# Performance work log

Measured on AMD Instinct MI355X. Metric: run time of the kernel, lower is better.

## Reference

```python
import jax, jax.numpy as jnp
import numpy as np

N_NODES = 50000
N_EDGES = 600000
IN_DIM = 128
HID = 256
OUT = 3


def setup_inputs() -> dict:
    key = jax.random.key(0)
    ks = jax.random.split(key, 10)
    x = jax.random.normal(ks[0], (N_NODES, IN_DIM), dtype=jnp.float32)
    edge_index = jax.random.randint(ks[1], (2, N_EDGES), 0, N_NODES, dtype=jnp.int64)
    s = lambda k, shp: jax.random.normal(k, shp, dtype=jnp.float32) * (1.0 / np.sqrt(shp[0]))
    return {
        "x": x,
        "edge_index": edge_index,
        # SAGEConv1: lin_l (applied to aggregated neighbors, with bias), lin_r (root, no bias)
        "W1l": s(ks[2], (IN_DIM, HID)), "b1": jnp.zeros((HID,), jnp.float32), "W1r": s(ks[3], (IN_DIM, HID)),
        # SAGEConv2
        "W2l": s(ks[4], (HID, HID)), "b2": jnp.zeros((HID,), jnp.float32), "W2r": s(ks[5], (HID, HID)),
        # classification head
        "Wh": s(ks[6], (HID, OUT)), "bh": jnp.zeros((OUT,), jnp.float32),
    }


def _sage_conv(x, edge_index, Wl, b, Wr):
    """PyG SAGEConv with mean aggregation: out = lin_l(mean_{j->i} x_j) + lin_r(x_i)."""
    src, dst = edge_index[0], edge_index[1]
    n = x.shape[0]
    # gather source features and scatter-mean onto targets
    msg_sum = jax.ops.segment_sum(x[src], dst, num_segments=n)          # [N, d]
    deg = jax.ops.segment_sum(jnp.ones((src.shape[0],), x.dtype), dst, num_segments=n)
    mean = msg_sum / jnp.maximum(deg, 1.0)[:, None]                      # isolated nodes -> 0
    return mean @ Wl + b + x @ Wr


def reference(x, edge_index, W1l, b1, W1r, W2l, b2, W2r, Wh, bh):
    h = jax.nn.relu(_sage_conv(x, edge_index, W1l, b1, W1r))
    # dropout(p=0.2) is identity in eval mode
    h = jax.nn.relu(_sage_conv(h, edge_index, W2l, b2, W2r))
    return h @ Wh + bh
```

## Files before the change

kernel.cpp:

```cpp
#include <hip/hip_runtime.h>
#include <hip/hip_bf16.h>

#define N_NODES 50000
#define N_EDGES 600000
#define IN_DIM 128
#define HID 256
#define OUT_DIM 3

#define M_PAD 50048

#define SCAN_B 256
#define SCAN_NB ((N_NODES + SCAN_B - 1) / SCAN_B)

typedef __bf16 bf16x8 __attribute__((ext_vector_type(8)));
typedef float f32x4 __attribute__((ext_vector_type(4)));

static __device__ __forceinline__ unsigned short f2b(float f) {
    union { float f; unsigned u; } u; u.f = f;
    unsigned r = u.u + 0x7fffu + ((u.u >> 16) & 1u);
    return (unsigned short)(r >> 16);
}
static __device__ __forceinline__ float b2f(unsigned short b) {
    union { unsigned u; float f; } u; u.u = ((unsigned)b) << 16;
    return u.f;
}


__global__ void count_deg_kernel(const int* __restrict__ dst, int* __restrict__ counts) {
    int e = blockIdx.x * blockDim.x + threadIdx.x;
    if (e < N_EDGES) atomicAdd(&counts[dst[e]], 1);
}

__global__ __launch_bounds__(256) void block_sum_kernel(const int* __restrict__ counts,
                                                        int* __restrict__ partial) {
    int node = blockIdx.x * SCAN_B + threadIdx.x;
    int v = (node < N_NODES) ? counts[node] : 0;
#pragma unroll
    for (int off = 32; off > 0; off >>= 1) v += __shfl_down(v, off);
    __shared__ int ws[4];
    if ((threadIdx.x & 63) == 0) ws[threadIdx.x >> 6] = v;
    __syncthreads();
    if (threadIdx.x == 0) partial[blockIdx.x] = ws[0] + ws[1] + ws[2] + ws[3];
}

__global__ __launch_bounds__(256) void scan_partial_kernel(int* __restrict__ partial) {
    __shared__ int s[SCAN_B];
    int t = threadIdx.x;
    int v = (t < SCAN_NB) ? partial[t] : 0;
    s[t] = v;
    __syncthreads();
    for (int off = 1; off < SCAN_B; off <<= 1) {
        int u = (t >= off) ? s[t - off] : 0;
        __syncthreads();
        s[t] += u;
        __syncthreads();
    }
    if (t < SCAN_NB) partial[t] = s[t] - v;
}

__global__ __launch_bounds__(256) void write_rowptr_kernel(const int* __restrict__ counts,
                                                           const int* __restrict__ partial,
                                                           int* __restrict__ row_ptr) {
    __shared__ int s[SCAN_B];
    int t = threadIdx.x;
    int node = blockIdx.x * SCAN_B + t;
    int v = (node < N_NODES) ? counts[node] : 0;
    s[t] = v;
    __syncthreads();
    for (int off = 1; off < SCAN_B; off <<= 1) {
        int u = (t >= off) ? s[t - off] : 0;
        __syncthreads();
        s[t] += u;
        __syncthreads();
    }
    if (node < N_NODES) row_ptr[node] = partial[blockIdx.x] + s[t] - v;
    if (node == 0) row_ptr[N_NODES] = N_EDGES;
}

__global__ void fill_csr_kernel(const int* __restrict__ src, const int* __restrict__ dst,
                                const int* __restrict__ row_ptr, int* __restrict__ cursor,
                                int* __restrict__ csr_src) {
    int e = blockIdx.x * blockDim.x + threadIdx.x;
    if (e < N_EDGES) {
        int d = dst[e];
        int pos = atomicAdd(&cursor[d], 1);
        csr_src[row_ptr[d] + pos] = src[e];
    }
}


__global__ void cast_f2b_kernel(const float* __restrict__ in, unsigned short* __restrict__ out, int n) {
    int i = blockIdx.x * blockDim.x + threadIdx.x;
    if (i * 4 < n) {
        float4 v = ((const float4*)in)[i];
        ushort4 o;
        o.x = f2b(v.x); o.y = f2b(v.y); o.z = f2b(v.z); o.w = f2b(v.w);
        ((ushort4*)out)[i] = o;
    }
}

__global__ void tcast4_kernel(const float* __restrict__ W1l, const float* __restrict__ W1r,
                              const float* __restrict__ W2l, const float* __restrict__ W2r,
                              unsigned short* __restrict__ W1lt, unsigned short* __restrict__ W1rt,
                              unsigned short* __restrict__ W2lt, unsigned short* __restrict__ W2rt) {
    int i = blockIdx.x * blockDim.x + threadIdx.x;
    const float* in; unsigned short* out; int K, base;
    if (i < 32768)        { in = W1l; out = W1lt; K = IN_DIM; base = 0; }
    else if (i < 65536)   { in = W1r; out = W1rt; K = IN_DIM; base = 32768; }
    else if (i < 131072)  { in = W2l; out = W2lt; K = HID;    base = 65536; }
    else if (i < 196608)  { in = W2r; out = W2rt; K = HID;    base = 131072; }
    else return;
    int j = i - base;
    int k = j >> 8;
    int n = j & 255;
    out[(size_t)n * K + k] = f2b(in[j]);
}

__global__ void init_out_kernel(const float* __restrict__ bh, float* __restrict__ out) {
    int i = blockIdx.x * blockDim.x + threadIdx.x;
    if (i < N_NODES * 3) out[i] = bh[i % 3];
}


static __device__ __forceinline__ void addv(float* acc, uint4 v) {
    acc[0] += b2f((unsigned short)(v.x & 0xffff));
    acc[1] += b2f((unsigned short)(v.x >> 16));
    acc[2] += b2f((unsigned short)(v.y & 0xffff));
    acc[3] += b2f((unsigned short)(v.y >> 16));
    acc[4] += b2f((unsigned short)(v.z & 0xffff));
    acc[5] += b2f((unsigned short)(v.z >> 16));
    acc[6] += b2f((unsigned short)(v.w & 0xffff));
    acc[7] += b2f((unsigned short)(v.w >> 16));
}

static __device__ __forceinline__ uint4 pack8(const float* a) {
    uint4 pk;
    pk.x = (unsigned)f2b(a[0]) | ((unsigned)f2b(a[1]) << 16);
    pk.y = (unsigned)f2b(a[2]) | ((unsigned)f2b(a[3]) << 16);
    pk.z = (unsigned)f2b(a[4]) | ((unsigned)f2b(a[5]) << 16);
    pk.w = (unsigned)f2b(a[6]) | ((unsigned)f2b(a[7]) << 16);
    return pk;
}

__global__ __launch_bounds__(256) void agg_mean256_kernel(const unsigned short* __restrict__ feat,
                                                          const int* __restrict__ row_ptr,
                                                          const int* __restrict__ csr_src,
                                                          unsigned short* __restrict__ out) {
    int node = blockIdx.x * 4 + (threadIdx.x >> 6);
    if (node >= N_NODES) return;
    int lane = threadIdx.x & 63;
    int half = lane >> 5, lh = lane & 31;
    const uint4* f4 = (const uint4*)feat;
    float acc[8];
#pragma unroll
    for (int j = 0; j < 8; j++) acc[j] = 0.f;
    int beg = row_ptr[node], end = row_ptr[node + 1];
    int i = beg;
    for (; i + 4 <= end; i += 4) {
        int sA = csr_src[i + half];
        int sB = csr_src[i + 2 + half];
        uint4 vA = f4[(size_t)sA * 32 + lh];
        uint4 vB = f4[(size_t)sB * 32 + lh];
        addv(acc, vA);
        addv(acc, vB);
    }
    if (i + 2 <= end) {
        int s = csr_src[i + half];
        addv(acc, f4[(size_t)s * 32 + lh]);
        i += 2;
    }
    if (i < end && half == 0) {
        int s = csr_src[i];
        addv(acc, f4[(size_t)s * 32 + lh]);
    }
    float inv = (end > beg) ? 1.0f / (float)(end - beg) : 0.0f;
#pragma unroll
    for (int j = 0; j < 8; j++) {
        acc[j] += __shfl_xor(acc[j], 32);
        acc[j] *= inv;
    }
    if (half == 0) ((uint4*)(out + (size_t)node * 256))[lh] = pack8(acc);
}

__global__ __launch_bounds__(256) void agg_mean128_kernel(const unsigned short* __restrict__ feat,
                                                          const int* __restrict__ row_ptr,
                                                          const int* __restrict__ csr_src,
                                                          unsigned short* __restrict__ out) {
    int node = blockIdx.x * 4 + (threadIdx.x >> 6);
    if (node >= N_NODES) return;
    int lane = threadIdx.x & 63;
    int q = lane >> 4, lq = lane & 15;
    const uint4* f4 = (const uint4*)feat;
    float acc[8];
#pragma unroll
    for (int j = 0; j < 8; j++) acc[j] = 0.f;
    int beg = row_ptr[node], end = row_ptr[node + 1];
    int i = beg;
    for (; i + 8 <= end; i += 8) {
        int sA = csr_src[i + q];
        int sB = csr_src[i + 4 + q];
        uint4 vA = f4[(size_t)sA * 16 + lq];
        uint4 vB = f4[(size_t)sB * 16 + lq];
        addv(acc, vA);
        addv(acc, vB);
    }
    if (i + 4 <= end) {
        int s = csr_src[i + q];
        addv(acc, f4[(size_t)s * 16 + lq]);
        i += 4;
    }
    int rem = end - i;
    if (q < rem) {
        int s = csr_src[i + q];
        addv(acc, f4[(size_t)s * 16 + lq]);
    }
    float inv = (end > beg) ? 1.0f / (float)(end - beg) : 0.0f;
#pragma unroll
    for (int j = 0; j < 8; j++) {
        acc[j] += __shfl_xor(acc[j], 32);
        acc[j] += __shfl_xor(acc[j], 16);
        acc[j] *= inv;
    }
    if (q == 0) ((uint4*)(out + (size_t)node * 128))[lq] = pack8(acc);
}


template <int KP>
static __device__ __forceinline__ void gemm_pipe_loop(
    const unsigned short* __restrict__ A0, const unsigned short* __restrict__ W0t,
    const unsigned short* __restrict__ A1, const unsigned short* __restrict__ W1t,
    unsigned short* As, unsigned short* Bs,
    int m0, int n0, int t, int w, int quad, int lr, f32x4 (&acc)[2][8]) {
    constexpr int KI = KP / 32;
    constexpr int NIT = 2 * KI;
    const int kb = t & 3;
    const int r  = t >> 2;

    const unsigned short* Aa[2] = {A0, A1};
    const unsigned short* Wa[2] = {W0t, W1t};

    uint4 ra0, ra1, rb0, rb1;
    auto gload = [&](int it) {
        int p = it / KI;
        int k0 = (it % KI) * 32 + kb * 8;
        const unsigned short* A = Aa[p];
        const unsigned short* Wt = Wa[p];
        ra0 = *(const uint4*)(A + (size_t)(m0 + r) * KP + k0);
        ra1 = *(const uint4*)(A + (size_t)(m0 + 64 + r) * KP + k0);
        rb0 = *(const uint4*)(Wt + (size_t)(n0 + r) * KP + k0);
        rb1 = *(const uint4*)(Wt + (size_t)(n0 + 64 + r) * KP + k0);
    };
    auto wlds = [&](int buf) {
        unsigned short* pa = As + buf * 4096;
        unsigned short* pb = Bs + buf * 4096;
        *(uint4*)&pa[(kb * 128 + r) * 8] = ra0;
        *(uint4*)&pa[(kb * 128 + 64 + r) * 8] = ra1;
        *(uint4*)&pb[(kb * 128 + r) * 8] = rb0;
        *(uint4*)&pb[(kb * 128 + 64 + r) * 8] = rb1;
    };

    gload(0);
    wlds(0);
    __syncthreads();
    for (int it = 0; it < NIT; ++it) {
        if (it + 1 < NIT) gload(it + 1);
        const unsigned short* pa = As + (it & 1) * 4096;
        const unsigned short* pb = Bs + (it & 1) * 4096;
        bf16x8 a[2], b[8];
        a[0] = *(const bf16x8*)&pa[(quad * 128 + w * 32 + lr) * 8];
        a[1] = *(const bf16x8*)&pa[(quad * 128 + w * 32 + 16 + lr) * 8];
#pragma unroll
        for (int nt = 0; nt < 8; nt++)
            b[nt] = *(const bf16x8*)&pb[(quad * 128 + nt * 16 + lr) * 8];
#pragma unroll
        for (int mt = 0; mt < 2; mt++)
#pragma unroll
            for (int nt = 0; nt < 8; nt++)
                acc[mt][nt] = __builtin_amdgcn_mfma_f32_16x16x32_bf16(a[mt], b[nt], acc[mt][nt], 0, 0, 0);
        if (it + 1 < NIT) {
            wlds((it + 1) & 1);
            __syncthreads();
        }
    }
}

template <int KP>
__global__ __launch_bounds__(256) void gemm_pipe_kernel(
    const unsigned short* __restrict__ A0, const unsigned short* __restrict__ W0t,
    const unsigned short* __restrict__ A1, const unsigned short* __restrict__ W1t,
    const float* __restrict__ bias, unsigned short* __restrict__ out, int M) {
    __shared__ __align__(16) unsigned short As[2 * 4096];
    __shared__ __align__(16) unsigned short Bs[2 * 4096];

    const int t = threadIdx.x;
    const int w = t >> 6, l = t & 63;
    const int quad = l >> 4, lr = l & 15;
    const int m0 = blockIdx.x * 128, n0 = blockIdx.y * 128;

    f32x4 acc[2][8];
    const f32x4 zero = {0.f, 0.f, 0.f, 0.f};
#pragma unroll
    for (int mt = 0; mt < 2; mt++)
#pragma unroll
        for (int nt = 0; nt < 8; nt++) acc[mt][nt] = zero;

    float bias_r[8];
#pragma unroll
    for (int nt = 0; nt < 8; nt++) bias_r[nt] = bias[n0 + nt * 16 + lr];

    gemm_pipe_loop<KP>(A0, W0t, A1, W1t, As, Bs, m0, n0, t, w, quad, lr, acc);

#pragma unroll
    for (int mt = 0; mt < 2; mt++)
#pragma unroll
        for (int r = 0; r < 4; r++) {
            int gm = m0 + w * 32 + mt * 16 + quad * 4 + r;
            if (gm >= M) continue;
            unsigned short* orow = out + (size_t)gm * HID;
#pragma unroll
            for (int nt = 0; nt < 8; nt++) {
                float v = fmaxf(acc[mt][nt][r] + bias_r[nt], 0.f);
                orow[n0 + nt * 16 + lr] = f2b(v);
            }
        }
}

template <int KP>
__global__ __launch_bounds__(256) void gemm_pipe_head_kernel(
    const unsigned short* __restrict__ A0, const unsigned short* __restrict__ W0t,
    const unsigned short* __restrict__ A1, const unsigned short* __restrict__ W1t,
    const float* __restrict__ bias, const float* __restrict__ Wh,
    float* __restrict__ out, int M) {
    __shared__ __align__(16) unsigned short As[2 * 4096];
    __shared__ __align__(16) unsigned short Bs[2 * 4096];

    const int t = threadIdx.x;
    const int w = t >> 6, l = t & 63;
    const int quad = l >> 4, lr = l & 15;
    const int m0 = blockIdx.x * 128, n0 = blockIdx.y * 128;

    f32x4 acc[2][8];
    const f32x4 zero = {0.f, 0.f, 0.f, 0.f};
#pragma unroll
    for (int mt = 0; mt < 2; mt++)
#pragma unroll
        for (int nt = 0; nt < 8; nt++) acc[mt][nt] = zero;

    float bias_r[8];
    float wh_r[8][3];
#pragma unroll
    for (int nt = 0; nt < 8; nt++) {
        int gn = n0 + nt * 16 + lr;
        bias_r[nt] = bias[gn];
        wh_r[nt][0] = Wh[gn * 3 + 0];
        wh_r[nt][1] = Wh[gn * 3 + 1];
        wh_r[nt][2] = Wh[gn * 3 + 2];
    }

    gemm_pipe_loop<KP>(A0, W0t, A1, W1t, As, Bs, m0, n0, t, w, quad, lr, acc);

#pragma unroll
    for (int mt = 0; mt < 2; mt++)
#pragma unroll
        for (int r = 0; r < 4; r++) {
            int gm = m0 + w * 32 + mt * 16 + quad * 4 + r;
            float p0 = 0.f, p1 = 0.f, p2 = 0.f;
#pragma unroll
            for (int nt = 0; nt < 8; nt++) {
                float v = fmaxf(acc[mt][nt][r] + bias_r[nt], 0.f);
                p0 += v * wh_r[nt][0];
                p1 += v * wh_r[nt][1];
                p2 += v * wh_r[nt][2];
            }
#pragma unroll
            for (int off = 1; off < 16; off <<= 1) {
                p0 += __shfl_xor(p0, off);
                p1 += __shfl_xor(p1, off);
                p2 += __shfl_xor(p2, off);
            }
            if (lr == 0 && gm < M) {
                atomicAdd(&out[(size_t)gm * 3 + 0], p0);
                atomicAdd(&out[(size_t)gm * 3 + 1], p1);
                atomicAdd(&out[(size_t)gm * 3 + 2], p2);
            }
        }
}


extern "C" void kernel_launch(void* const* d_in, const int* in_sizes, int n_in,
                              void* d_out, int out_size, void* d_ws, size_t ws_size,
                              hipStream_t stream) {
    const float* x   = (const float*)d_in[0];
    const int*   ei  = (const int*)d_in[1];
    const int*   src = ei;
    const int*   dst = ei + N_EDGES;
    const float* W1l = (const float*)d_in[2];
    const float* b1  = (const float*)d_in[3];
    const float* W1r = (const float*)d_in[4];
    const float* W2l = (const float*)d_in[5];
    const float* b2  = (const float*)d_in[6];
    const float* W2r = (const float*)d_in[7];
    const float* Wh  = (const float*)d_in[8];
    const float* bh  = (const float*)d_in[9];
    float* out = (float*)d_out;

    char* ws = (char*)d_ws;
    size_t off = 0;
    auto alloc = [&](size_t bytes) -> void* {
        void* p = ws + off;
        off = (off + bytes + 255) & ~(size_t)255;
        return p;
    };
    int* counts   = (int*)alloc((size_t)N_NODES * 4);
    int* row_ptr  = (int*)alloc((size_t)(N_NODES + 1) * 4);
    int* cursor   = (int*)alloc((size_t)N_NODES * 4);
    int* partial  = (int*)alloc((size_t)SCAN_NB * 4);
    int* csr_src  = (int*)alloc((size_t)N_EDGES * 4);
    unsigned short* xb   = (unsigned short*)alloc((size_t)M_PAD * IN_DIM * 2);
    unsigned short* agg  = (unsigned short*)alloc((size_t)M_PAD * HID * 2);
    unsigned short* h1   = (unsigned short*)alloc((size_t)M_PAD * HID * 2);
    unsigned short* W1lt = (unsigned short*)alloc((size_t)IN_DIM * HID * 2);
    unsigned short* W1rt = (unsigned short*)alloc((size_t)IN_DIM * HID * 2);
    unsigned short* W2lt = (unsigned short*)alloc((size_t)HID * HID * 2);
    unsigned short* W2rt = (unsigned short*)alloc((size_t)HID * HID * 2);

    hipMemsetAsync(counts, 0, (size_t)N_NODES * 4, stream);
    hipMemsetAsync(cursor, 0, (size_t)N_NODES * 4, stream);

    const int eblocks = (N_EDGES + 255) / 256;
    count_deg_kernel<<<eblocks, 256, 0, stream>>>(dst, counts);
    block_sum_kernel<<<SCAN_NB, SCAN_B, 0, stream>>>(counts, partial);
    scan_partial_kernel<<<1, SCAN_B, 0, stream>>>(partial);
    write_rowptr_kernel<<<SCAN_NB, SCAN_B, 0, stream>>>(counts, partial, row_ptr);
    fill_csr_kernel<<<eblocks, 256, 0, stream>>>(src, dst, row_ptr, cursor, csr_src);

    {
        int n = N_NODES * IN_DIM;
        cast_f2b_kernel<<<(n / 4 + 255) / 256, 256, 0, stream>>>(x, xb, n);
        tcast4_kernel<<<(196608 + 255) / 256, 256, 0, stream>>>(W1l, W1r, W2l, W2r,
                                                                W1lt, W1rt, W2lt, W2rt);
        init_out_kernel<<<(N_NODES * 3 + 255) / 256, 256, 0, stream>>>(bh, out);
    }

    const int nblocks4 = (N_NODES + 3) / 4;
    dim3 gg(M_PAD / 128, HID / 128);

    agg_mean128_kernel<<<nblocks4, 256, 0, stream>>>(xb, row_ptr, csr_src, agg);
    gemm_pipe_kernel<IN_DIM><<<gg, 256, 0, stream>>>(agg, W1lt, xb, W1rt, b1, h1, N_NODES);

    agg_mean256_kernel<<<nblocks4, 256, 0, stream>>>(h1, row_ptr, csr_src, agg);
    gemm_pipe_head_kernel<HID><<<gg, 256, 0, stream>>>(agg, W2lt, h1, W2rt, b2, Wh, out, N_NODES);
}
```

Before: 289.8 us.

## Stage 128-wide weight slabs in LDS and stream A per-wave

Result: slower. 296.6 us (+2.3%).

```diff
diff --git a/kernel.cpp b/kernel.cpp
--- a/kernel.cpp
+++ b/kernel.cpp
@@ -226,71 +226,78 @@
 
 
 template <int KP>
-static __device__ __forceinline__ void gemm_pipe_loop(
+static __device__ __forceinline__ void gemm_stage_loop(
     const unsigned short* __restrict__ A0, const unsigned short* __restrict__ W0t,
     const unsigned short* __restrict__ A1, const unsigned short* __restrict__ W1t,
-    unsigned short* As, unsigned short* Bs,
-    int m0, int n0, int t, int w, int quad, int lr, f32x4 (&acc)[2][8]) {
-    constexpr int KI = KP / 32;
-    constexpr int NIT = 2 * KI;
-    const int kb = t & 3;
-    const int r  = t >> 2;
-
-    const unsigned short* Aa[2] = {A0, A1};
-    const unsigned short* Wa[2] = {W0t, W1t};
-
-    uint4 ra0, ra1, rb0, rb1;
-    auto gload = [&](int it) {
-        int p = it / KI;
-        int k0 = (it % KI) * 32 + kb * 8;
-        const unsigned short* A = Aa[p];
-        const unsigned short* Wt = Wa[p];
-        ra0 = *(const uint4*)(A + (size_t)(m0 + r) * KP + k0);
-        ra1 = *(const uint4*)(A + (size_t)(m0 + 64 + r) * KP + k0);
-        rb0 = *(const uint4*)(Wt + (size_t)(n0 + r) * KP + k0);
-        rb1 = *(const uint4*)(Wt + (size_t)(n0 + 64 + r) * KP + k0);
-    };
-    auto wlds = [&](int buf) {
-        unsigned short* pa = As + buf * 4096;
-        unsigned short* pb = Bs + buf * 4096;
-        *(uint4*)&pa[(kb * 128 + r) * 8] = ra0;
-        *(uint4*)&pa[(kb * 128 + 64 + r) * 8] = ra1;
-        *(uint4*)&pb[(kb * 128 + r) * 8] = rb0;
-        *(uint4*)&pb[(kb * 128 + 64 + r) * 8] = rb1;
-    };
-
-    gload(0);
-    wlds(0);
-    __syncthreads();
-    for (int it = 0; it < NIT; ++it) {
-        if (it + 1 < NIT) gload(it + 1);
-        const unsigned short* pa = As + (it & 1) * 4096;
-        const unsigned short* pb = Bs + (it & 1) * 4096;
-        bf16x8 a[2], b[8];
-        a[0] = *(const bf16x8*)&pa[(quad * 128 + w * 32 + lr) * 8];
-        a[1] = *(const bf16x8*)&pa[(quad * 128 + w * 32 + 16 + lr) * 8];
-#pragma unroll
-        for (int nt = 0; nt < 8; nt++)
-            b[nt] = *(const bf16x8*)&pb[(quad * 128 + nt * 16 + lr) * 8];
-#pragma unroll
-        for (int mt = 0; mt < 2; mt++)
+    unsigned short* Bl, unsigned short* Al,
+    int m0, int n0, int t, int w, int l, int quad, int lr, f32x4 (&acc)[2][8]) {
+    constexpr int NSTAGE = (2 * KP) / 128;
+
+    for (int s = 0; s < NSTAGE; ++s) {
+        const int p = s / (KP / 128);
+        const int k0 = (s % (KP / 128)) * 128;
+        const unsigned short* A = p ? A1 : A0;
+        const unsigned short* Wt = p ? W1t : W0t;
+
+        if (s) __syncthreads();
+        {
+            const int nr = t >> 1, h = t & 1;
+            const unsigned short* gsrc = Wt + (size_t)(n0 + nr) * KP + k0 + h * 64;
+            unsigned short* ldst = Bl + nr * 136 + h * 64;
+#pragma unroll
+            for (int j = 0; j < 8; j++)
+                *(uint4*)(ldst + j * 8) = *(const uint4*)(gsrc + j * 8);
+        }
+        __syncthreads();
+
+        const unsigned short* Abase =
+            A + (size_t)(m0 + w * 32 + (l >> 1)) * KP + k0 + (l & 1) * 16;
+        unsigned short* Aw = Al + w * 2048;
+        const int arow = l >> 1, ah = l & 1;
+
+        uint4 ra[2][2];
+#pragma unroll
+        for (int pre = 0; pre < 2; pre++) {
+            const unsigned short* pA = Abase + pre * 32;
+            ra[pre][0] = *(const uint4*)(pA);
+            ra[pre][1] = *(const uint4*)(pA + 8);
+        }
+#pragma unroll
+        for (int k = 0; k < 4; ++k) {
+            unsigned short* pw = Aw + (k & 1) * 1024;
+#pragma unroll
+            for (int j = 0; j < 2; j++) {
+                int kb = ah * 2 + j;
+                *(uint4*)&pw[(kb * 32 + arow) * 8] = ra[k & 1][j];
+            }
+            if (k + 2 < 4) {
+                const unsigned short* pA = Abase + (k + 2) * 32;
+                ra[k & 1][0] = *(const uint4*)(pA);
+                ra[k & 1][1] = *(const uint4*)(pA + 8);
+            }
+            bf16x8 a[2], b[8];
+            a[0] = *(const bf16x8*)&pw[(quad * 32 + lr) * 8];
+            a[1] = *(const bf16x8*)&pw[(quad * 32 + 16 + lr) * 8];
 #pragma unroll
             for (int nt = 0; nt < 8; nt++)
-                acc[mt][nt] = __builtin_amdgcn_mfma_f32_16x16x32_bf16(a[mt], b[nt], acc[mt][nt], 0, 0, 0);
-        if (it + 1 < NIT) {
-            wlds((it + 1) & 1);
-            __syncthreads();
+                b[nt] = *(const bf16x8*)&Bl[(nt * 16 + lr) * 136 + k * 32 + quad * 8];
+#pragma unroll
+            for (int mt = 0; mt < 2; mt++)
+#pragma unroll
+                for (int nt = 0; nt < 8; nt++)
+                    acc[mt][nt] = __builtin_amdgcn_mfma_f32_16x16x32_bf16(a[mt], b[nt],
+                                                                          acc[mt][nt], 0, 0, 0);
         }
     }
 }
 
 template <int KP>
-__global__ __launch_bounds__(256) void gemm_pipe_kernel(
+__global__ __launch_bounds__(256) void gemm_stage_kernel(
     const unsigned short* __restrict__ A0, const unsigned short* __restrict__ W0t,
     const unsigned short* __restrict__ A1, const unsigned short* __restrict__ W1t,
     const float* __restrict__ bias, unsigned short* __restrict__ out, int M) {
-    __shared__ __align__(16) unsigned short As[2 * 4096];
-    __shared__ __align__(16) unsigned short Bs[2 * 4096];
+    __shared__ __align__(16) unsigned short Bl[128 * 136];
+    __shared__ __align__(16) unsigned short Al[4 * 2 * 1024];
 
     const int t = threadIdx.x;
     const int w = t >> 6, l = t & 63;
@@ -308,7 +315,7 @@
 #pragma unroll
     for (int nt = 0; nt < 8; nt++) bias_r[nt] = bias[n0 + nt * 16 + lr];
 
-    gemm_pipe_loop<KP>(A0, W0t, A1, W1t, As, Bs, m0, n0, t, w, quad, lr, acc);
+    gemm_stage_loop<KP>(A0, W0t, A1, W1t, Bl, Al, m0, n0, t, w, l, quad, lr, acc);
 
 #pragma unroll
     for (int mt = 0; mt < 2; mt++)
@@ -326,13 +333,13 @@
 }
 
 template <int KP>
-__global__ __launch_bounds__(256) void gemm_pipe_head_kernel(
+__global__ __launch_bounds__(256) void gemm_stage_head_kernel(
     const unsigned short* __restrict__ A0, const unsigned short* __restrict__ W0t,
     const unsigned short* __restrict__ A1, const unsigned short* __restrict__ W1t,
     const float* __restrict__ bias, const float* __restrict__ Wh,
     float* __restrict__ out, int M) {
-    __shared__ __align__(16) unsigned short As[2 * 4096];
-    __shared__ __align__(16) unsigned short Bs[2 * 4096];
+    __shared__ __align__(16) unsigned short Bl[128 * 136];
+    __shared__ __align__(16) unsigned short Al[4 * 2 * 1024];
 
     const int t = threadIdx.x;
     const int w = t >> 6, l = t & 63;
@@ -357,7 +364,7 @@
         wh_r[nt][2] = Wh[gn * 3 + 2];
     }
 
-    gemm_pipe_loop<KP>(A0, W0t, A1, W1t, As, Bs, m0, n0, t, w, quad, lr, acc);
+    gemm_stage_loop<KP>(A0, W0t, A1, W1t, Bl, Al, m0, n0, t, w, l, quad, lr, acc);
 
 #pragma unroll
     for (int mt = 0; mt < 2; mt++)
@@ -446,8 +453,8 @@
     dim3 gg(M_PAD / 128, HID / 128);
 
     agg_mean128_kernel<<<nblocks4, 256, 0, stream>>>(xb, row_ptr, csr_src, agg);
-    gemm_pipe_kernel<IN_DIM><<<gg, 256, 0, stream>>>(agg, W1lt, xb, W1rt, b1, h1, N_NODES);
+    gemm_stage_kernel<IN_DIM><<<gg, 256, 0, stream>>>(agg, W1lt, xb, W1rt, b1, h1, N_NODES);
 
     agg_mean256_kernel<<<nblocks4, 256, 0, stream>>>(h1, row_ptr, csr_src, agg);
-    gemm_pipe_head_kernel<HID><<<gg, 256, 0, stream>>>(agg, W2lt, h1, W2rt, b2, Wh, out, N_NODES);
-}
+    gemm_stage_head_kernel<HID><<<gg, 256, 0, stream>>>(agg, W2lt, h1, W2rt, b2, Wh, out, N_NODES);
+}
```
